# Performance work log

Measured on AMD Instinct MI355X. Metric: run time of the kernel, lower is better.

The kernel has to match this reference:

```python
import jax, jax.numpy as jnp
import numpy as np

N, E, F_IN, HID, H, G = 50000, 800000, 128, 128, 4, 64
D = HID // H  # per-head dim = 32


def setup_inputs() -> dict:
    key = jax.random.key(0)
    ks = jax.random.split(key, 24)
    s = 0.05
    x = jax.random.normal(ks[0], (N, F_IN), dtype=jnp.float32)
    edge_index = jax.random.randint(ks[1], (2, E), 0, N, dtype=jnp.int64)
    batch = jnp.sort(jax.random.randint(ks[2], (N,), 0, G, dtype=jnp.int64))
    p = {}
    # layer 1: in F_IN -> H*D, layer 2: in HID -> H*D; each conv has q,k,v,skip linears (bias=True)
    names = ['Wq1', 'Wk1', 'Wv1', 'Ws1', 'Wq2', 'Wk2', 'Wv2', 'Ws2']
    dims = [(F_IN, HID)] * 4 + [(HID, HID)] * 4
    for i, (nm, dm) in enumerate(zip(names, dims)):
        p[nm] = jax.random.normal(ks[3 + 2 * i], dm, dtype=jnp.float32) * s
        p['b' + nm[1:]] = jax.random.normal(ks[4 + 2 * i], (dm[1],), dtype=jnp.float32) * s
    p['Wfc'] = jax.random.normal(ks[20], (HID, 1), dtype=jnp.float32) * s
    p['bfc'] = jax.random.normal(ks[21], (1,), dtype=jnp.float32) * s
    return {'x': x, 'edge_index': edge_index, 'batch': batch, **p}


def transformer_conv(x, edge_index, Wq, bq, Wk, bk, Wv, bv, Ws, bs):
    src, dst = edge_index[0], edge_index[1]  # messages flow src -> dst
    q = (x @ Wq + bq).reshape(-1, H, D)[dst]          # [E,H,D]
    k = (x @ Wk + bk).reshape(-1, H, D)[src]          # [E,H,D]
    v = (x @ Wv + bv).reshape(-1, H, D)[src]          # [E,H,D]
    logits = jnp.einsum('ehd,ehd->eh', q, k) / jnp.sqrt(jnp.float32(D))  # [E,H]
    m = jax.ops.segment_max(logits, dst, num_segments=N)                 # [N,H]
    e = jnp.exp(logits - m[dst])
    s = jax.ops.segment_sum(e, dst, num_segments=N)                      # [N,H]
    alpha = e / s[dst]
    agg = jax.ops.segment_sum(alpha[..., None] * v, dst, num_segments=N)  # [N,H,D]
    return agg.reshape(-1, HID) + (x @ Ws + bs)


def reference(x, edge_index, batch, Wq1, bq1, Wk1, bk1, Wv1, bv1, Ws1, bs1,
              Wq2, bq2, Wk2, bk2, Wv2, bv2, Ws2, bs2, Wfc, bfc):
    h = jax.nn.relu(transformer_conv(x, edge_index, Wq1, bq1, Wk1, bk1, Wv1, bv1, Ws1, bs1))
    h = jax.nn.relu(transformer_conv(h, edge_index, Wq2, bq2, Wk2, bk2, Wv2, bv2, Ws2, bs2))
    sums = jax.ops.segment_sum(h, batch, num_segments=G)                 # [G,HID]
    cnt = jax.ops.segment_sum(jnp.ones((h.shape[0],), h.dtype), batch, num_segments=G)
    pooled = sums / jnp.maximum(cnt, 1.0)[:, None]
    return (pooled @ Wfc + bfc).squeeze(-1)
```

## Files before the change

### kernel.cpp

```cpp
#include <hip/hip_runtime.h>
#include <hip/hip_bf16.h>
#include <math.h>

#define HID 128

typedef __attribute__((ext_vector_type(8))) short short8;
typedef __attribute__((ext_vector_type(4))) short short4v;
typedef __attribute__((ext_vector_type(4))) float f32x4;
typedef __attribute__((ext_vector_type(2))) float f32x2;
typedef __attribute__((ext_vector_type(4))) int int4v;
typedef __attribute__((ext_vector_type(4))) unsigned short ushort4v;
typedef __attribute__((ext_vector_type(2))) unsigned short ushort2v;

static inline size_t align256(size_t x){ return (x + 255) & ~(size_t)255; }

__device__ inline float bf2f(unsigned short h) {
  union { unsigned u; float f; } uf; uf.u = ((unsigned)h) << 16; return uf.f;
}
__device__ inline unsigned short f2bf(float f) {
  union { float f; unsigned u; } uf; uf.f = f;
  unsigned r = uf.u + 0x7fff + ((uf.u >> 16) & 1);
  return (unsigned short)(r >> 16);
}

__device__ inline float dpp_rsum16(float x) {
  int v;
  v = __builtin_amdgcn_update_dpp(0, __float_as_int(x), 0xB1, 0xF, 0xF, true);
  x += __int_as_float(v);
  v = __builtin_amdgcn_update_dpp(0, __float_as_int(x), 0x4E, 0xF, 0xF, true);
  x += __int_as_float(v);
  v = __builtin_amdgcn_update_dpp(0, __float_as_int(x), 0x124, 0xF, 0xF, true);
  x += __int_as_float(v);
  v = __builtin_amdgcn_update_dpp(0, __float_as_int(x), 0x128, 0xF, 0xF, true);
  x += __int_as_float(v);
  return x;
}

__global__ __launch_bounds__(256) void k_prep(
    const float* W0, const float* W1, const float* W2, const float* W3,
    const float* W4, const float* W5, const float* W6, const float* W7,
    const float* b0, const float* b1, const float* b2, const float* b3,
    const float* b4, const float* b5, const float* b6, const float* b7,
    unsigned short* Wcat, float* Bcat,
    const int* __restrict__ edst, int* __restrict__ deg, int e)
{
  __shared__ float tl[32][33];
  if (blockIdx.x >= 128) {
    for (int i = (blockIdx.x - 128) * 256 + threadIdx.x; i < e; i += 512 * 256)
      atomicAdd(&deg[edst[i]], 1);
    return;
  }
  const float* Ws[8] = {W0, W1, W2, W3, W4, W5, W6, W7};
  const float* bs[8] = {b0, b1, b2, b3, b4, b5, b6, b7};
  int m = blockIdx.x >> 4, tile = blockIdx.x & 15;
  int tr = (tile >> 2) * 32, tc = (tile & 3) * 32;
  int tx = threadIdx.x & 31, ty = threadIdx.x >> 5;
  const float* Wm = Ws[m];
  #pragma unroll
  for (int r = 0; r < 32; r += 8) tl[ty + r][tx] = Wm[(tr + ty + r) * 128 + tc + tx];
  __syncthreads();
  #pragma unroll
  for (int r = 0; r < 32; r += 8)
    Wcat[m * 16384 + (tc + ty + r) * 128 + tr + tx] = f2bf(tl[tx][ty + r]);
  if (tile == 0 && threadIdx.x < 128) Bcat[m * 128 + threadIdx.x] = bs[m][threadIdx.x];
}

__global__ void k_scan_a(const int* __restrict__ deg, int* __restrict__ rowptr,
                         int* __restrict__ bsum, int n) {
  __shared__ int tmp[512];
  int t = threadIdx.x, i = blockIdx.x * 512 + t;
  int v = (i < n) ? deg[i] : 0;
  tmp[t] = v;
  __syncthreads();
  for (int off = 1; off < 512; off <<= 1) {
    int u = (t >= off) ? tmp[t - off] : 0;
    __syncthreads();
    tmp[t] += u;
    __syncthreads();
  }
  if (i < n) rowptr[i] = tmp[t] - v;
  if (t == 511) bsum[blockIdx.x] = tmp[t];
}

__global__ void k_scan_c(int* __restrict__ rowptr, int* __restrict__ cursor,
                         const int* __restrict__ bsum, int n, int e, int nb) {
  __shared__ int sred[8];
  __shared__ int base_sh;
  int t = threadIdx.x;
  int v = (t < nb && t < (int)blockIdx.x) ? bsum[t] : 0;
  #pragma unroll
  for (int off = 32; off >= 1; off >>= 1) v += __shfl_xor(v, off);
  if ((t & 63) == 0) sred[t >> 6] = v;
  __syncthreads();
  if (t == 0) {
    int b = 0;
    #pragma unroll
    for (int j = 0; j < 8; ++j) b += sred[j];
    base_sh = b;
  }
  __syncthreads();
  int base = base_sh;
  int i = blockIdx.x * 512 + t;
  if (i < n) { int val = rowptr[i] + base; rowptr[i] = val; cursor[i] = val; }
  if (i == 0) rowptr[n] = e;
}

template<int ABF16>
__device__ __forceinline__ void qkvs_body(
    int bx, const void* __restrict__ Ain, const unsigned short* __restrict__ Wl,
    const float* __restrict__ Bl, unsigned short* __restrict__ Qb,
    unsigned short* __restrict__ KVb, float* __restrict__ Sb, int n,
    unsigned short* sA, unsigned short* sW)
{
  const int tid = threadIdx.x;
  const int rb = bx * 64;

  if (ABF16) {
    const unsigned short* A = (const unsigned short*)Ain;
    #pragma unroll
    for (int it = 0; it < 4; ++it) {
      int q = tid + it * 256;
      int row = q >> 4, ch = q & 15;
      int gr = rb + row;
      short8 h = {0,0,0,0,0,0,0,0};
      if (gr < n) h = *reinterpret_cast<const short8*>(A + (size_t)gr * HID + ch * 8);
      *reinterpret_cast<short8*>(&sA[row * 128 + ((ch ^ (row & 7)) << 3)]) = h;
    }
  } else {
    const float* A = (const float*)Ain;
    #pragma unroll
    for (int it = 0; it < 8; ++it) {
      int q = tid + it * 256;
      int row = q >> 5, c4 = (q & 31) * 4;
      int gr = rb + row;
      f32x4 a = {0.f, 0.f, 0.f, 0.f};
      if (gr < n) a = *reinterpret_cast<const f32x4*>(A + (size_t)gr * HID + c4);
      short4v h;
      h.x = (short)f2bf(a.x); h.y = (short)f2bf(a.y);
      h.z = (short)f2bf(a.z); h.w = (short)f2bf(a.w);
      int eloff = row * 128 + (((c4 >> 3) ^ (row & 7)) << 3) + (c4 & 7);
      *reinterpret_cast<short4v*>(&sA[eloff]) = h;
    }
  }

  const int lane = tid & 63;
  const int wv = tid >> 6;

  auto stageW = [&](int y) {
    const unsigned short* Wy = Wl + (size_t)y * 16384;
    #pragma unroll
    for (int it = 0; it < 8; ++it) {
      int q = tid + it * 256;
      int c = q >> 4, ch = q & 15;
      short8 w = *reinterpret_cast<const short8*>(Wy + c * 128 + ch * 8);
      *reinterpret_cast<short8*>(&sW[c * 128 + ((ch ^ (c & 7)) << 3)]) = w;
    }
  };

  stageW(0);
  __syncthreads();

  short8 af[4];
  #pragma unroll
  for (int ks = 0; ks < 4; ++ks) {
    int ch = ks * 4 + (lane >> 4);
    int row = wv * 16 + (lane & 15);
    af[ks] = *reinterpret_cast<const short8*>(&sA[row * 128 + ((ch ^ (row & 7)) << 3)]);
  }

  f32x4 acc[8];
  auto compute = [&]() {
    #pragma unroll
    for (int mf = 0; mf < 8; ++mf) acc[mf] = (f32x4){0.f, 0.f, 0.f, 0.f};
    #pragma unroll
    for (int ks = 0; ks < 4; ++ks) {
      int ch = ks * 4 + (lane >> 4);
      short8 wf[8];
      #pragma unroll
      for (int mf = 0; mf < 8; ++mf) {
        int wc = mf * 16 + (lane & 15);
        wf[mf] = *reinterpret_cast<const short8*>(&sW[wc * 128 + ((ch ^ (wc & 7)) << 3)]);
      }
      #pragma unroll
      for (int mf = 0; mf < 8; ++mf)
        acc[mf] = __builtin_amdgcn_mfma_f32_16x16x32_bf16(wf[mf], af[ks], acc[mf], 0, 0, 0);
    }
  };

  const int gr = rb + wv * 16 + (lane & 15);
  const int cbase = (lane >> 4) << 2;

  compute();
  if (gr < n) {
    #pragma unroll
    for (int mf = 0; mf < 8; ++mf) {
      int c0 = mf * 16 + cbase;
      f32x4 b = *reinterpret_cast<const f32x4*>(Bl + 0 * 128 + c0);
      f32x4 v = acc[mf];
      short4v h;
      h.x = (short)f2bf(v.x + b.x); h.y = (short)f2bf(v.y + b.y);
      h.z = (short)f2bf(v.z + b.z); h.w = (short)f2bf(v.w + b.w);
      *reinterpret_cast<short4v*>(Qb + (size_t)gr * HID + c0) = h;
    }
  }

  __syncthreads();
  stageW(3);
  __syncthreads();
  compute();
  if (gr < n) {
    #pragma unroll
    for (int mf = 0; mf < 8; ++mf) {
      int c0 = mf * 16 + cbase;
      f32x4 b = *reinterpret_cast<const f32x4*>(Bl + 3 * 128 + c0);
      f32x4 v = acc[mf];
      v.x += b.x; v.y += b.y; v.z += b.z; v.w += b.w;
      *reinterpret_cast<f32x4*>(Sb + (size_t)gr * HID + c0) = v;
    }
  }

  __syncthreads();
  stageW(1);
  __syncthreads();
  compute();
  f32x4 kacc[8];
  #pragma unroll
  for (int mf = 0; mf < 8; ++mf) kacc[mf] = acc[mf];

  __syncthreads();
  stageW(2);
  __syncthreads();
  compute();
  if (gr < n) {
    #pragma unroll
    for (int mf = 0; mf < 8; ++mf) {
      int c0 = mf * 16 + cbase;
      f32x4 bk = *reinterpret_cast<const f32x4*>(Bl + 1 * 128 + c0);
      f32x4 bv = *reinterpret_cast<const f32x4*>(Bl + 2 * 128 + c0);
      f32x4 kv = kacc[mf], vv = acc[mf];
      short8 h;
      h[0] = (short)f2bf(kv.x + bk.x); h[1] = (short)f2bf(kv.y + bk.y);
      h[2] = (short)f2bf(vv.x + bv.x); h[3] = (short)f2bf(vv.y + bv.y);
      h[4] = (short)f2bf(kv.z + bk.z); h[5] = (short)f2bf(kv.w + bk.w);
      h[6] = (short)f2bf(vv.z + bv.z); h[7] = (short)f2bf(vv.w + bv.w);
      *reinterpret_cast<short8*>(KVb + (size_t)gr * 256 + 2 * c0) = h;
    }
  }
}

__global__ __launch_bounds__(256, 2) void k_scat_qkvs1(
    const int* __restrict__ srcA, const int* __restrict__ dstA,
    int* __restrict__ cursor, int* __restrict__ csrc, int e,
    const void* __restrict__ Ain, const unsigned short* __restrict__ Wl,
    const float* __restrict__ Bl, unsigned short* __restrict__ Qb,
    unsigned short* __restrict__ KVb, float* __restrict__ Sb, int n)
{
  __shared__ unsigned short sA[64 * 128];
  __shared__ unsigned short sW[128 * 128];
  if (blockIdx.x < 512) {
    for (int i = blockIdx.x * 256 + threadIdx.x; i < e; i += 512 * 256) {
      int pos = atomicAdd(&cursor[dstA[i]], 1);
      csrc[pos] = srcA[i] << 9;
    }
    return;
  }
  qkvs_body<0>(blockIdx.x - 512, Ain, Wl, Bl, Qb, KVb, Sb, n, sA, sW);
}

__global__ __launch_bounds__(256, 2) void k_qkvs2(
    const void* __restrict__ Ain, const unsigned short* __restrict__ Wl,
    const float* __restrict__ Bl, unsigned short* __restrict__ Qb,
    unsigned short* __restrict__ KVb, float* __restrict__ Sb, int n)
{
  __shared__ unsigned short sA[64 * 128];
  __shared__ unsigned short sW[128 * 128];
  qkvs_body<1>(blockIdx.x, Ain, Wl, Bl, Qb, KVb, Sb, n, sA, sW);
}

__global__ __launch_bounds__(256) void k_attn2(
    const unsigned short* __restrict__ Qb, const unsigned short* __restrict__ KVb,
    const float* __restrict__ Sb, const int* __restrict__ rowptr,
    const int* __restrict__ csrc, unsigned short* __restrict__ Hout, int n)
{
  int wid = blockIdx.x * 4 + (threadIdx.x >> 6);
  if (wid >= n) return;
  int lane = threadIdx.x & 63;
  ushort2v qv = *reinterpret_cast<const ushort2v*>(Qb + (size_t)wid * HID + 2 * lane);
  const float sc = 0.25503487f;
  float q0 = bf2f(qv.x) * sc, q1 = bf2f(qv.y) * sc;
  int e0 = rowptr[wid], deg = rowptr[wid + 1] - e0;
  const int* cp = csrc + e0;
  const char* kvb = (const char*)KVb + lane * 8;
  float m = -INFINITY, s = 0.f, a0 = 0.f, a1 = 0.f;

  auto LDo = [&](int off) -> ushort4v {
    return *reinterpret_cast<const ushort4v*>(kvb + (unsigned)off);
  };
  auto proc1 = [&](ushort4v kv) {
    float d = q0 * bf2f(kv.x) + q1 * bf2f(kv.y);
    float lg = dpp_rsum16(d);
    if (!__all(lg <= m + 11.5f)) {
      float nm = fmaxf(m, lg);
      float cc = __builtin_amdgcn_exp2f(m - nm);
      s *= cc; a0 *= cc; a1 *= cc; m = nm;
    }
    float p = __builtin_amdgcn_exp2f(lg - m);
    s += p;
    a0 = fmaf(p, bf2f(kv.z), a0);
    a1 = fmaf(p, bf2f(kv.w), a1);
  };
  auto proc4 = [&](ushort4v e0v, ushort4v e1v, ushort4v e2v, ushort4v e3v) {
    float d0 = q0 * bf2f(e0v.x) + q1 * bf2f(e0v.y);
    float d1 = q0 * bf2f(e1v.x) + q1 * bf2f(e1v.y);
    float d2 = q0 * bf2f(e2v.x) + q1 * bf2f(e2v.y);
    float d3 = q0 * bf2f(e3v.x) + q1 * bf2f(e3v.y);
    float l0 = dpp_rsum16(d0), l1 = dpp_rsum16(d1);
    float l2 = dpp_rsum16(d2), l3 = dpp_rsum16(d3);
    float qm = fmaxf(fmaxf(l0, l1), fmaxf(l2, l3));
    if (!__all(qm <= m + 11.5f)) {
      float nm = fmaxf(m, qm);
      float cc = __builtin_amdgcn_exp2f(m - nm);
      s *= cc; a0 *= cc; a1 *= cc; m = nm;
    }
    float p0 = __builtin_amdgcn_exp2f(l0 - m);
    float p1 = __builtin_amdgcn_exp2f(l1 - m);
    float p2 = __builtin_amdgcn_exp2f(l2 - m);
    float p3 = __builtin_amdgcn_exp2f(l3 - m);
    s += (p0 + p1) + (p2 + p3);
    a0 = fmaf(p3, bf2f(e3v.z), fmaf(p2, bf2f(e2v.z), fmaf(p1, bf2f(e1v.z), fmaf(p0, bf2f(e0v.z), a0))));
    a1 = fmaf(p3, bf2f(e3v.w), fmaf(p2, bf2f(e2v.w), fmaf(p1, bf2f(e1v.w), fmaf(p0, bf2f(e0v.w), a1))));
  };

  int nq = deg >> 2, r = deg & 3;
  if (nq) {
    int4v o; __builtin_memcpy(&o, cp, 16);
    ushort4v b0 = LDo(o.x), b1 = LDo(o.y), b2 = LDo(o.z), b3 = LDo(o.w);
    for (int q = 1; q < nq; ++q) {
      int4v no; __builtin_memcpy(&no, cp + 4 * q, 16);
      ushort4v n0 = LDo(no.x), n1 = LDo(no.y), n2 = LDo(no.z), n3 = LDo(no.w);
      proc4(b0, b1, b2, b3);
      b0 = n0; b1 = n1; b2 = n2; b3 = n3;
    }
    proc4(b0, b1, b2, b3);
  }
  int tb = nq * 4;
  for (int i = 0; i < r; ++i) proc1(LDo(cp[tb + i]));

  float inv = (s > 0.f) ? 1.f / s : 0.f;
  f32x2 sv = *reinterpret_cast<const f32x2*>(Sb + (size_t)wid * HID + 2 * lane);
  ushort2v h;
  h.x = f2bf(fmaxf(a0 * inv + sv.x, 0.f));
  h.y = f2bf(fmaxf(a1 * inv + sv.y, 0.f));
  *reinterpret_cast<ushort2v*>(Hout + (size_t)wid * HID + 2 * lane) = h;
}

__global__ __launch_bounds__(256) void k_poolfc(
    const unsigned short* __restrict__ H, const int* __restrict__ batch,
    const float* __restrict__ Wfc, const float* __restrict__ bfc,
    float* __restrict__ out, int n)
{
  int g = blockIdx.x;
  int lo = 0, hi = n;
  while (lo < hi) { int mid = (lo + hi) >> 1; if (batch[mid] < g) lo = mid + 1; else hi = mid; }
  int start = lo;
  hi = n;
  while (lo < hi) { int mid = (lo + hi) >> 1; if (batch[mid] < g + 1) lo = mid + 1; else hi = mid; }
  int end = lo;

  int t = threadIdx.x;
  int col = t & 127, rr = t >> 7;
  float a0 = 0.f, a1 = 0.f, a2 = 0.f, a3 = 0.f;
  int i = start + rr;
  for (; i + 6 < end; i += 8) {
    a0 += bf2f(H[(size_t)i * HID + col]);
    a1 += bf2f(H[(size_t)(i + 2) * HID + col]);
    a2 += bf2f(H[(size_t)(i + 4) * HID + col]);
    a3 += bf2f(H[(size_t)(i + 6) * HID + col]);
  }
  for (; i < end; i += 2) a0 += bf2f(H[(size_t)i * HID + col]);
  float v = ((a0 + a1) + (a2 + a3)) * Wfc[col];

  __shared__ float red[4];
  #pragma unroll
  for (int off = 32; off >= 1; off >>= 1) v += __shfl_xor(v, off);
  if ((t & 63) == 0) red[t >> 6] = v;
  __syncthreads();
  if (t == 0) {
    float tot = (red[0] + red[1]) + (red[2] + red[3]);
    float cnt = (float)(end - start);
    out[g] = tot / fmaxf(cnt, 1.f) + bfc[0];
  }
}

extern "C" void kernel_launch(void* const* d_in, const int* in_sizes, int n_in,
                              void* d_out, int out_size, void* d_ws, size_t ws_size,
                              hipStream_t stream)
{
  const float* x   = (const float*)d_in[0];
  const int*   ei  = (const int*)d_in[1];
  const int*   bat = (const int*)d_in[2];
  const float *Wq1 = (const float*)d_in[3],  *bq1 = (const float*)d_in[4];
  const float *Wk1 = (const float*)d_in[5],  *bk1 = (const float*)d_in[6];
  const float *Wv1 = (const float*)d_in[7],  *bv1 = (const float*)d_in[8];
  const float *Ws1 = (const float*)d_in[9],  *bs1 = (const float*)d_in[10];
  const float *Wq2 = (const float*)d_in[11], *bq2 = (const float*)d_in[12];
  const float *Wk2 = (const float*)d_in[13], *bk2 = (const float*)d_in[14];
  const float *Wv2 = (const float*)d_in[15], *bv2 = (const float*)d_in[16];
  const float *Ws2 = (const float*)d_in[17], *bs2 = (const float*)d_in[18];
  const float *Wfc = (const float*)d_in[19], *bfc = (const float*)d_in[20];
  float* out = (float*)d_out;

  const int N = in_sizes[0] / HID;
  const int E = in_sizes[1] / 2;
  const int G = 64;

  char* p = (char*)d_ws;
  auto alloc = [&](size_t bytes) -> char* { char* r = p; p += align256(bytes); return r; };
  unsigned short* Qb  = (unsigned short*)alloc((size_t)N * HID * 2);
  unsigned short* KVb = (unsigned short*)alloc((size_t)N * 256 * 2);
  float* Sb   = (float*)alloc((size_t)N * HID * 4);
  unsigned short* Hb  = (unsigned short*)alloc((size_t)N * HID * 2);
  unsigned short* H2b = (unsigned short*)alloc((size_t)N * HID * 2);
  unsigned short* Wcat = (unsigned short*)alloc((size_t)8 * 128 * 128 * 2);
  float* Bcat = (float*)alloc((size_t)8 * 128 * 4);
  int* rowptr = (int*)alloc((size_t)(N + 1) * sizeof(int));
  int* cursor = (int*)alloc((size_t)N * sizeof(int));
  int* deg    = (int*)alloc((size_t)N * sizeof(int));
  int* bsum   = (int*)alloc(4096);
  int* csrc   = (int*)alloc((size_t)E * sizeof(int));

  const int* esrc = ei;
  const int* edst = ei + E;

  hipMemsetAsync(deg, 0, (size_t)N * sizeof(int), stream);

  k_prep<<<640, 256, 0, stream>>>(Wq1, Wk1, Wv1, Ws1, Wq2, Wk2, Wv2, Ws2,
                                  bq1, bk1, bv1, bs1, bq2, bk2, bv2, bs2,
                                  Wcat, Bcat, edst, deg, E);
  int SB = (N + 511) / 512;
  k_scan_a<<<SB, 512, 0, stream>>>(deg, rowptr, bsum, N);
  k_scan_c<<<SB, 512, 0, stream>>>(rowptr, cursor, bsum, N, E, SB);

  int QB = (N + 63) / 64;
  k_scat_qkvs1<<<512 + QB, 256, 0, stream>>>(esrc, edst, cursor, csrc, E,
                                             x, Wcat, Bcat, Qb, KVb, Sb, N);
  k_attn2<<<(N + 3) / 4, 256, 0, stream>>>(Qb, KVb, Sb, rowptr, csrc, Hb, N);
  k_qkvs2<<<QB, 256, 0, stream>>>(Hb, Wcat + 4 * 16384, Bcat + 512, Qb, KVb, Sb, N);
  k_attn2<<<(N + 3) / 4, 256, 0, stream>>>(Qb, KVb, Sb, rowptr, csrc, H2b, N);
  k_poolfc<<<G, 256, 0, stream>>>(H2b, bat, Wfc, bfc, out, N);
}
```

Baseline: 398.3 us.

## Use fp16 storage with fdot2, LDS-histogram CSR build, fp16 skip buffer

After: 743.4 us. +86.6%, slower.

```diff
diff --git a/kernel.cpp b/kernel.cpp
--- a/kernel.cpp
+++ b/kernel.cpp
@@ -9,18 +9,23 @@
 typedef __attribute__((ext_vector_type(4))) float f32x4;
 typedef __attribute__((ext_vector_type(2))) float f32x2;
 typedef __attribute__((ext_vector_type(4))) int int4v;
+typedef __attribute__((ext_vector_type(2))) unsigned int uint2v;
 typedef __attribute__((ext_vector_type(4))) unsigned short ushort4v;
 typedef __attribute__((ext_vector_type(2))) unsigned short ushort2v;
+typedef __attribute__((ext_vector_type(2))) _Float16 half2v;
 
 static inline size_t align256(size_t x){ return (x + 255) & ~(size_t)255; }
 
-__device__ inline float bf2f(unsigned short h) {
-  union { unsigned u; float f; } uf; uf.u = ((unsigned)h) << 16; return uf.f;
-}
 __device__ inline unsigned short f2bf(float f) {
   union { float f; unsigned u; } uf; uf.f = f;
   unsigned r = uf.u + 0x7fff + ((uf.u >> 16) & 1);
   return (unsigned short)(r >> 16);
+}
+__device__ inline unsigned short f2h(float f) {
+  union { _Float16 h; unsigned short u; } c; c.h = (_Float16)f; return c.u;
+}
+__device__ inline half2v b2h2(unsigned u) {
+  union { unsigned u; half2v h; } c; c.u = u; return c.h;
 }
 
 __device__ inline float dpp_rsum16(float x) {
@@ -36,40 +41,53 @@
   return x;
 }
 
-__global__ __launch_bounds__(256) void k_prep(
+__global__ __launch_bounds__(512) void k_prep(
     const float* W0, const float* W1, const float* W2, const float* W3,
     const float* W4, const float* W5, const float* W6, const float* W7,
     const float* b0, const float* b1, const float* b2, const float* b3,
     const float* b4, const float* b5, const float* b6, const float* b7,
     unsigned short* Wcat, float* Bcat,
-    const int* __restrict__ edst, int* __restrict__ deg, int e)
+    const int* __restrict__ edst, int* __restrict__ degA, int* __restrict__ degB, int e)
 {
   __shared__ float tl[32][33];
+  __shared__ int hh[512];
+  int t = threadIdx.x;
   if (blockIdx.x >= 128) {
-    for (int i = (blockIdx.x - 128) * 256 + threadIdx.x; i < e; i += 512 * 256)
-      atomicAdd(&deg[edst[i]], 1);
+    int hb = blockIdx.x - 128;
+    int chunk = hb >> 1, half = hb & 1;
+    int lo = chunk << 9;
+    hh[t] = 0;
+    __syncthreads();
+    int eh = e >> 1;
+    int i0 = half ? eh : 0, i1 = half ? e : eh;
+    for (int i = i0 + t; i < i1; i += 512) {
+      unsigned u = (unsigned)(edst[i] - lo);
+      if (u < 512u) atomicAdd(&hh[u], 1);
+    }
+    __syncthreads();
+    (half ? degB : degA)[lo + t] = hh[t];
     return;
   }
   const float* Ws[8] = {W0, W1, W2, W3, W4, W5, W6, W7};
   const float* bs[8] = {b0, b1, b2, b3, b4, b5, b6, b7};
   int m = blockIdx.x >> 4, tile = blockIdx.x & 15;
   int tr = (tile >> 2) * 32, tc = (tile & 3) * 32;
-  int tx = threadIdx.x & 31, ty = threadIdx.x >> 5;
+  int tx = t & 31, ty = t >> 5;
   const float* Wm = Ws[m];
   #pragma unroll
-  for (int r = 0; r < 32; r += 8) tl[ty + r][tx] = Wm[(tr + ty + r) * 128 + tc + tx];
-  __syncthreads();
-  #pragma unroll
-  for (int r = 0; r < 32; r += 8)
+  for (int r = 0; r < 32; r += 16) tl[ty + r][tx] = Wm[(tr + ty + r) * 128 + tc + tx];
+  __syncthreads();
+  #pragma unroll
+  for (int r = 0; r < 32; r += 16)
     Wcat[m * 16384 + (tc + ty + r) * 128 + tr + tx] = f2bf(tl[tx][ty + r]);
-  if (tile == 0 && threadIdx.x < 128) Bcat[m * 128 + threadIdx.x] = bs[m][threadIdx.x];
-}
-
-__global__ void k_scan_a(const int* __restrict__ deg, int* __restrict__ rowptr,
-                         int* __restrict__ bsum, int n) {
+  if (tile == 0 && t < 128) Bcat[m * 128 + t] = bs[m][t];
+}
+
+__global__ void k_scan_a(const int* __restrict__ degA, const int* __restrict__ degB,
+                         int* __restrict__ rowptr, int* __restrict__ bsum, int n) {
   __shared__ int tmp[512];
   int t = threadIdx.x, i = blockIdx.x * 512 + t;
-  int v = (i < n) ? deg[i] : 0;
+  int v = (i < n) ? degA[i] + degB[i] : 0;
   tmp[t] = v;
   __syncthreads();
   for (int off = 1; off < 512; off <<= 1) {
@@ -82,8 +100,8 @@
   if (t == 511) bsum[blockIdx.x] = tmp[t];
 }
 
-__global__ void k_scan_c(int* __restrict__ rowptr, int* __restrict__ cursor,
-                         const int* __restrict__ bsum, int n, int e, int nb) {
+__global__ void k_scan_c(int* __restrict__ rowptr, const int* __restrict__ bsum,
+                         int n, int e, int nb) {
   __shared__ int sred[8];
   __shared__ int base_sh;
   int t = threadIdx.x;
@@ -99,21 +117,50 @@
     base_sh = b;
   }
   __syncthreads();
-  int base = base_sh;
   int i = blockIdx.x * 512 + t;
-  if (i < n) { int val = rowptr[i] + base; rowptr[i] = val; cursor[i] = val; }
+  if (i < n) rowptr[i] += base_sh;
   if (i == 0) rowptr[n] = e;
 }
 
+__global__ __launch_bounds__(512) void k_scatter(
+    const int* __restrict__ esrc, const int* __restrict__ edst,
+    const int* __restrict__ rowptr, const int* __restrict__ degA,
+    int* __restrict__ csrc, int e, int n)
+{
+  __shared__ int cur[512];
+  int t = threadIdx.x;
+  int chunk = blockIdx.x >> 1, half = blockIdx.x & 1;
+  int lo = chunk << 9;
+  int idx = lo + t;
+  int base = 0;
+  if (idx < n) {
+    base = rowptr[idx];
+    if (half) base += degA[idx];
+  }
+  cur[t] = base;
+  __syncthreads();
+  int eh = e >> 1;
+  int i0 = half ? eh : 0, i1 = half ? e : eh;
+  for (int i = i0 + t; i < i1; i += 512) {
+    unsigned u = (unsigned)(edst[i] - lo);
+    if (u < 512u) {
+      int pos = atomicAdd(&cur[u], 1);
+      csrc[pos] = esrc[i] << 9;
+    }
+  }
+}
+
 template<int ABF16>
-__device__ __forceinline__ void qkvs_body(
-    int bx, const void* __restrict__ Ain, const unsigned short* __restrict__ Wl,
+__global__ __launch_bounds__(256, 3) void k_qkvs(
+    const void* __restrict__ Ain, const unsigned short* __restrict__ Wl,
     const float* __restrict__ Bl, unsigned short* __restrict__ Qb,
-    unsigned short* __restrict__ KVb, float* __restrict__ Sb, int n,
-    unsigned short* sA, unsigned short* sW)
-{
+    unsigned short* __restrict__ KVb, unsigned short* __restrict__ Sb, int n)
+{
+  __shared__ unsigned short sA[64 * 128];
+  __shared__ unsigned short sW[128 * 128];
   const int tid = threadIdx.x;
-  const int rb = bx * 64;
+  const int rb = blockIdx.x * 64;
+  const float QSC = 0.25503487f;
 
   if (ABF16) {
     const unsigned short* A = (const unsigned short*)Ain;
@@ -197,10 +244,10 @@
       int c0 = mf * 16 + cbase;
       f32x4 b = *reinterpret_cast<const f32x4*>(Bl + 0 * 128 + c0);
       f32x4 v = acc[mf];
-      short4v h;
-      h.x = (short)f2bf(v.x + b.x); h.y = (short)f2bf(v.y + b.y);
-      h.z = (short)f2bf(v.z + b.z); h.w = (short)f2bf(v.w + b.w);
-      *reinterpret_cast<short4v*>(Qb + (size_t)gr * HID + c0) = h;
+      ushort4v h;
+      h.x = f2h((v.x + b.x) * QSC); h.y = f2h((v.y + b.y) * QSC);
+      h.z = f2h((v.z + b.z) * QSC); h.w = f2h((v.w + b.w) * QSC);
+      *reinterpret_cast<ushort4v*>(Qb + (size_t)gr * HID + c0) = h;
     }
   }
 
@@ -214,8 +261,10 @@
       int c0 = mf * 16 + cbase;
       f32x4 b = *reinterpret_cast<const f32x4*>(Bl + 3 * 128 + c0);
       f32x4 v = acc[mf];
-      v.x += b.x; v.y += b.y; v.z += b.z; v.w += b.w;
-      *reinterpret_cast<f32x4*>(Sb + (size_t)gr * HID + c0) = v;
+      ushort4v h;
+      h.x = f2h(v.x + b.x); h.y = f2h(v.y + b.y);
+      h.z = f2h(v.z + b.z); h.w = f2h(v.w + b.w);
+      *reinterpret_cast<ushort4v*>(Sb + (size_t)gr * HID + c0) = h;
     }
   }
 
@@ -239,83 +288,50 @@
       f32x4 bv = *reinterpret_cast<const f32x4*>(Bl + 2 * 128 + c0);
       f32x4 kv = kacc[mf], vv = acc[mf];
       short8 h;
-      h[0] = (short)f2bf(kv.x + bk.x); h[1] = (short)f2bf(kv.y + bk.y);
-      h[2] = (short)f2bf(vv.x + bv.x); h[3] = (short)f2bf(vv.y + bv.y);
-      h[4] = (short)f2bf(kv.z + bk.z); h[5] = (short)f2bf(kv.w + bk.w);
-      h[6] = (short)f2bf(vv.z + bv.z); h[7] = (short)f2bf(vv.w + bv.w);
+      h[0] = (short)f2h(kv.x + bk.x); h[1] = (short)f2h(kv.y + bk.y);
+      h[2] = (short)f2h(vv.x + bv.x); h[3] = (short)f2h(vv.y + bv.y);
+      h[4] = (short)f2h(kv.z + bk.z); h[5] = (short)f2h(kv.w + bk.w);
+      h[6] = (short)f2h(vv.z + bv.z); h[7] = (short)f2h(vv.w + bv.w);
       *reinterpret_cast<short8*>(KVb + (size_t)gr * 256 + 2 * c0) = h;
     }
   }
 }
 
-__global__ __launch_bounds__(256, 2) void k_scat_qkvs1(
-    const int* __restrict__ srcA, const int* __restrict__ dstA,
-    int* __restrict__ cursor, int* __restrict__ csrc, int e,
-    const void* __restrict__ Ain, const unsigned short* __restrict__ Wl,
-    const float* __restrict__ Bl, unsigned short* __restrict__ Qb,
-    unsigned short* __restrict__ KVb, float* __restrict__ Sb, int n)
-{
-  __shared__ unsigned short sA[64 * 128];
-  __shared__ unsigned short sW[128 * 128];
-  if (blockIdx.x < 512) {
-    for (int i = blockIdx.x * 256 + threadIdx.x; i < e; i += 512 * 256) {
-      int pos = atomicAdd(&cursor[dstA[i]], 1);
-      csrc[pos] = srcA[i] << 9;
-    }
-    return;
-  }
-  qkvs_body<0>(blockIdx.x - 512, Ain, Wl, Bl, Qb, KVb, Sb, n, sA, sW);
-}
-
-__global__ __launch_bounds__(256, 2) void k_qkvs2(
-    const void* __restrict__ Ain, const unsigned short* __restrict__ Wl,
-    const float* __restrict__ Bl, unsigned short* __restrict__ Qb,
-    unsigned short* __restrict__ KVb, float* __restrict__ Sb, int n)
-{
-  __shared__ unsigned short sA[64 * 128];
-  __shared__ unsigned short sW[128 * 128];
-  qkvs_body<1>(blockIdx.x, Ain, Wl, Bl, Qb, KVb, Sb, n, sA, sW);
-}
-
-__global__ __launch_bounds__(256) void k_attn2(
+__global__ __launch_bounds__(256, 8) void k_attn2(
     const unsigned short* __restrict__ Qb, const unsigned short* __restrict__ KVb,
-    const float* __restrict__ Sb, const int* __restrict__ rowptr,
+    const unsigned short* __restrict__ Sb, const int* __restrict__ rowptr,
     const int* __restrict__ csrc, unsigned short* __restrict__ Hout, int n)
 {
   int wid = blockIdx.x * 4 + (threadIdx.x >> 6);
   if (wid >= n) return;
   int lane = threadIdx.x & 63;
-  ushort2v qv = *reinterpret_cast<const ushort2v*>(Qb + (size_t)wid * HID + 2 * lane);
-  const float sc = 0.25503487f;
-  float q0 = bf2f(qv.x) * sc, q1 = bf2f(qv.y) * sc;
+  half2v qh = b2h2(*reinterpret_cast<const unsigned*>(Qb + (size_t)wid * HID + 2 * lane));
   int e0 = rowptr[wid], deg = rowptr[wid + 1] - e0;
   const int* cp = csrc + e0;
   const char* kvb = (const char*)KVb + lane * 8;
   float m = -INFINITY, s = 0.f, a0 = 0.f, a1 = 0.f;
 
-  auto LDo = [&](int off) -> ushort4v {
-    return *reinterpret_cast<const ushort4v*>(kvb + (unsigned)off);
+  auto LDo = [&](int off) -> uint2v {
+    return *reinterpret_cast<const uint2v*>(kvb + (unsigned)off);
   };
-  auto proc1 = [&](ushort4v kv) {
-    float d = q0 * bf2f(kv.x) + q1 * bf2f(kv.y);
-    float lg = dpp_rsum16(d);
+  auto proc1 = [&](uint2v kv) {
+    float lg = dpp_rsum16(__builtin_amdgcn_fdot2(qh, b2h2(kv.x), 0.f, false));
     if (!__all(lg <= m + 11.5f)) {
       float nm = fmaxf(m, lg);
       float cc = __builtin_amdgcn_exp2f(m - nm);
       s *= cc; a0 *= cc; a1 *= cc; m = nm;
     }
     float p = __builtin_amdgcn_exp2f(lg - m);
+    half2v vh = b2h2(kv.y);
     s += p;
-    a0 = fmaf(p, bf2f(kv.z), a0);
-    a1 = fmaf(p, bf2f(kv.w), a1);
+    a0 = fmaf(p, (float)vh.x, a0);
+    a1 = fmaf(p, (float)vh.y, a1);
   };
-  auto proc4 = [&](ushort4v e0v, ushort4v e1v, ushort4v e2v, ushort4v e3v) {
-    float d0 = q0 * bf2f(e0v.x) + q1 * bf2f(e0v.y);
-    float d1 = q0 * bf2f(e1v.x) + q1 * bf2f(e1v.y);
-    float d2 = q0 * bf2f(e2v.x) + q1 * bf2f(e2v.y);
-    float d3 = q0 * bf2f(e3v.x) + q1 * bf2f(e3v.y);
-    float l0 = dpp_rsum16(d0), l1 = dpp_rsum16(d1);
-    float l2 = dpp_rsum16(d2), l3 = dpp_rsum16(d3);
+  auto proc4 = [&](uint2v e0v, uint2v e1v, uint2v e2v, uint2v e3v) {
+    float l0 = dpp_rsum16(__builtin_amdgcn_fdot2(qh, b2h2(e0v.x), 0.f, false));
+    float l1 = dpp_rsum16(__builtin_amdgcn_fdot2(qh, b2h2(e1v.x), 0.f, false));
+    float l2 = dpp_rsum16(__builtin_amdgcn_fdot2(qh, b2h2(e2v.x), 0.f, false));
+    float l3 = dpp_rsum16(__builtin_amdgcn_fdot2(qh, b2h2(e3v.x), 0.f, false));
     float qm = fmaxf(fmaxf(l0, l1), fmaxf(l2, l3));
     if (!__all(qm <= m + 11.5f)) {
       float nm = fmaxf(m, qm);
@@ -327,17 +343,18 @@
     float p2 = __builtin_amdgcn_exp2f(l2 - m);
     float p3 = __builtin_amdgcn_exp2f(l3 - m);
     s += (p0 + p1) + (p2 + p3);
-    a0 = fmaf(p3, bf2f(e3v.z), fmaf(p2, bf2f(e2v.z), fmaf(p1, bf2f(e1v.z), fmaf(p0, bf2f(e0v.z), a0))));
-    a1 = fmaf(p3, bf2f(e3v.w), fmaf(p2, bf2f(e2v.w), fmaf(p1, bf2f(e1v.w), fmaf(p0, bf2f(e0v.w), a1))));
+    half2v v0 = b2h2(e0v.y), v1 = b2h2(e1v.y), v2 = b2h2(e2v.y), v3 = b2h2(e3v.y);
+    a0 = fmaf(p3, (float)v3.x, fmaf(p2, (float)v2.x, fmaf(p1, (float)v1.x, fmaf(p0, (float)v0.x, a0))));
+    a1 = fmaf(p3, (float)v3.y, fmaf(p2, (float)v2.y, fmaf(p1, (float)v1.y, fmaf(p0, (float)v0.y, a1))));
   };
 
   int nq = deg >> 2, r = deg & 3;
   if (nq) {
     int4v o; __builtin_memcpy(&o, cp, 16);
-    ushort4v b0 = LDo(o.x), b1 = LDo(o.y), b2 = LDo(o.z), b3 = LDo(o.w);
+    uint2v b0 = LDo(o.x), b1 = LDo(o.y), b2 = LDo(o.z), b3 = LDo(o.w);
     for (int q = 1; q < nq; ++q) {
       int4v no; __builtin_memcpy(&no, cp + 4 * q, 16);
-      ushort4v n0 = LDo(no.x), n1 = LDo(no.y), n2 = LDo(no.z), n3 = LDo(no.w);
+      uint2v n0 = LDo(no.x), n1 = LDo(no.y), n2 = LDo(no.z), n3 = LDo(no.w);
       proc4(b0, b1, b2, b3);
       b0 = n0; b1 = n1; b2 = n2; b3 = n3;
     }
@@ -347,13 +364,16 @@
   for (int i = 0; i < r; ++i) proc1(LDo(cp[tb + i]));
 
   float inv = (s > 0.f) ? 1.f / s : 0.f;
-  f32x2 sv = *reinterpret_cast<const f32x2*>(Sb + (size_t)wid * HID + 2 * lane);
+  half2v sh = b2h2(*reinterpret_cast<const unsigned*>(Sb + (size_t)wid * HID + 2 * lane));
   ushort2v h;
-  h.x = f2bf(fmaxf(a0 * inv + sv.x, 0.f));
-  h.y = f2bf(fmaxf(a1 * inv + sv.y, 0.f));
+  h.x = f2bf(fmaxf(fmaf(a0, inv, (float)sh.x), 0.f));
+  h.y = f2bf(fmaxf(fmaf(a1, inv, (float)sh.y), 0.f));
   *reinterpret_cast<ushort2v*>(Hout + (size_t)wid * HID + 2 * lane) = h;
 }
 
+__device__ inline float bf2f(unsigned short h) {
+  union { unsigned u; float f; } uf; uf.u = ((unsigned)h) << 16; return uf.f;
+}
 __global__ __launch_bounds__(256) void k_poolfc(
     const unsigned short* __restrict__ H, const int* __restrict__ batch,
     const float* __restrict__ Wfc, const float* __restrict__ bfc,
@@ -413,39 +433,40 @@
   const int N = in_sizes[0] / HID;
   const int E = in_sizes[1] / 2;
   const int G = 64;
+  const int NCH = (N + 511) >> 9;
 
   char* p = (char*)d_ws;
   auto alloc = [&](size_t bytes) -> char* { char* r = p; p += align256(bytes); return r; };
   unsigned short* Qb  = (unsigned short*)alloc((size_t)N * HID * 2);
   unsigned short* KVb = (unsigned short*)alloc((size_t)N * 256 * 2);
-  float* Sb   = (float*)alloc((size_t)N * HID * 4);
+  unsigned short* Sb  = (unsigned short*)alloc((size_t)N * HID * 2);
   unsigned short* Hb  = (unsigned short*)alloc((size_t)N * HID * 2);
   unsigned short* H2b = (unsigned short*)alloc((size_t)N * HID * 2);
   unsigned short* Wcat = (unsigned short*)alloc((size_t)8 * 128 * 128 * 2);
   float* Bcat = (float*)alloc((size_t)8 * 128 * 4);
   int* rowptr = (int*)alloc((size_t)(N + 1) * sizeof(int));
-  int* cursor = (int*)alloc((size_t)N * sizeof(int));
-  int* deg    = (int*)alloc((size_t)N * sizeof(int));
+  int* degA   = (int*)alloc((size_t)NCH * 512 * sizeof(int));
+  int* degB   = (int*)alloc((size_t)NCH * 512 * sizeof(int));
   int* bsum   = (int*)alloc(4096);
   int* csrc   = (int*)alloc((size_t)E * sizeof(int));
 
   const int* esrc = ei;
   const int* edst = ei + E;
 
-  hipMemsetAsync(deg, 0, (size_t)N * sizeof(int), stream);
-
-  k_prep<<<640, 256, 0, stream>>>(Wq1, Wk1, Wv1, Ws1, Wq2, Wk2, Wv2, Ws2,
-                                  bq1, bk1, bv1, bs1, bq2, bk2, bv2, bs2,
-                                  Wcat, Bcat, edst, deg, E);
+  k_prep<<<128 + 2 * NCH, 512, 0, stream>>>(
+      Wq1, Wk1, Wv1, Ws1, Wq2, Wk2, Wv2, Ws2,
+      bq1, bk1, bv1, bs1, bq2, bk2, bv2, bs2,
+      Wcat, Bcat, edst, degA, degB, E);
+
   int SB = (N + 511) / 512;
-  k_scan_a<<<SB, 512, 0, stream>>>(deg, rowptr, bsum, N);
-  k_scan_c<<<SB, 512, 0, stream>>>(rowptr, cursor, bsum, N, E, SB);
+  k_scan_a<<<SB, 512, 0, stream>>>(degA, degB, rowptr, bsum, N);
+  k_scan_c<<<SB, 512, 0, stream>>>(rowptr, bsum, N, E, SB);
+  k_scatter<<<2 * NCH, 512, 0, stream>>>(esrc, edst, rowptr, degA, csrc, E, N);
 
   int QB = (N + 63) / 64;
-  k_scat_qkvs1<<<512 + QB, 256, 0, stream>>>(esrc, edst, cursor, csrc, E,
-                                             x, Wcat, Bcat, Qb, KVb, Sb, N);
+  k_qkvs<0><<<QB, 256, 0, stream>>>(x, Wcat, Bcat, Qb, KVb, Sb, N);
   k_attn2<<<(N + 3) / 4, 256, 0, stream>>>(Qb, KVb, Sb, rowptr, csrc, Hb, N);
-  k_qkvs2<<<QB, 256, 0, stream>>>(Hb, Wcat + 4 * 16384, Bcat + 512, Qb, KVb, Sb, N);
+  k_qkvs<1><<<QB, 256, 0, stream>>>(Hb, Wcat + 4 * 16384, Bcat + 512, Qb, KVb, Sb, N);
   k_attn2<<<(N + 3) / 4, 256, 0, stream>>>(Qb, KVb, Sb, rowptr, csrc, H2b, N);
   k_poolfc<<<G, 256, 0, stream>>>(H2b, bat, Wfc, bfc, out, N);
 }
```
